# Optimization experiments

Measured on AMD Instinct MI355X. Metric: run time of the kernel, lower is better.

## Reference

```python
import jax, jax.numpy as jnp
import numpy as np

B, T, U, D = 8, 200, 50, 512
INNER, VOCAB = 640, 1024


def setup_inputs() -> dict:
    key = jax.random.key(0)
    k1, k2, k3, k4 = jax.random.split(key, 4)
    enc_outputs = jax.random.normal(k1, (B, T, D), dtype=jnp.float32)
    dec_outputs = jax.random.normal(k2, (B, U, D), dtype=jnp.float32)
    # Dense(inner_dim, activation='tanh') params
    W1 = jax.random.normal(k3, (D, INNER), dtype=jnp.float32) / np.sqrt(D)
    b1 = jnp.zeros((INNER,), dtype=jnp.float32)
    # Dense(vocab_size) params
    W2 = jax.random.normal(k4, (INNER, VOCAB), dtype=jnp.float32) / np.sqrt(INNER)
    b2 = jnp.zeros((VOCAB,), dtype=jnp.float32)
    return {"enc_outputs": enc_outputs, "dec_outputs": dec_outputs,
            "W1": W1, "b1": b1, "W2": W2, "b2": b2}


def reference(enc_outputs, dec_outputs, W1, b1, W2, b2):
    # joint_inputs: (B, T, U, D) via broadcast add, exactly as the TF module
    joint = enc_outputs[:, :, None, :] + dec_outputs[:, None, :, :]
    hidden = jnp.tanh(jnp.einsum('btud,dh->btuh', joint, W1) + b1)  # (B,T,U,INNER)
    logits = jnp.einsum('btuh,hv->btuv', hidden, W2) + b2            # (B,T,U,VOCAB)
    return logits
```

## Files before the change

kernel.cpp:

```cpp
#include <hip/hip_runtime.h>
#include <hip/hip_bf16.h>
#include <stdint.h>

namespace {

constexpr int B = 8, T = 200, U = 50, D = 512, INNER = 640, VOCAB = 1024;
constexpr int M_TOTAL = B * T * U;
constexpr int ROWS_E = B * T;
constexpr int ROWS_D = B * U;
constexpr int ROWS_ED = ROWS_E + ROWS_D;
constexpr int BM = 128, BN = 512;
constexpr int CK = 128;

typedef __bf16 bf16x8 __attribute__((ext_vector_type(8)));
typedef float  f32x4  __attribute__((ext_vector_type(4)));
typedef unsigned short u16;
typedef unsigned int   u32;

constexpr size_t ED_BYTES = (size_t)ROWS_ED * INNER * 4;

__device__ __forceinline__ u16 f2bf(float f) {
  uint32_t u = __float_as_uint(f);
  uint32_t rounding = 0x7FFFu + ((u >> 16) & 1u);
  return (u16)((u + rounding) >> 16);
}

__device__ __forceinline__ float fast_tanh(float x) {
  float e = __expf(2.0f * x);
  float r = __builtin_amdgcn_rcpf(e + 1.0f);
  return 1.0f - 2.0f * r;
}

__global__ __launch_bounds__(320) void k_prep(const float* __restrict__ enc,
                                              const float* __restrict__ dec,
                                              const float* __restrict__ W1,
                                              const float* __restrict__ b1,
                                              const float* __restrict__ W2,
                                              float* __restrict__ ED,
                                              u16* __restrict__ W2B) {
  if (blockIdx.x >= 500) {
    const int idx = (blockIdx.x - 500) * 320 + threadIdx.x;
    const int lane = idx & 63;
    const int f = idx >> 6;
    const int ks = f >> 6;
    const int nf = f & 63;
    const int n = nf * 16 + (lane & 15);
    const int k = ks * 32 + (lane >> 4) * 8;
    u16 v[8];
#pragma unroll
    for (int j = 0; j < 8; ++j)
      v[j] = f2bf(W2[(size_t)(k + j) * VOCAB + n]);
    uint64_t lo = (uint64_t)v[0] | ((uint64_t)v[1] << 16) |
                  ((uint64_t)v[2] << 32) | ((uint64_t)v[3] << 48);
    uint64_t hi = (uint64_t)v[4] | ((uint64_t)v[5] << 16) |
                  ((uint64_t)v[6] << 32) | ((uint64_t)v[7] << 48);
    uint64_t* dst = reinterpret_cast<uint64_t*>(W2B + (size_t)idx * 8);
    dst[0] = lo;
    dst[1] = hi;
    return;
  }

  __shared__ float rows[4 * D];
  const int r0 = blockIdx.x * 4;
  const bool is_enc = (r0 < ROWS_E);
  const float* src = is_enc ? (enc + (size_t)r0 * D)
                            : (dec + (size_t)(r0 - ROWS_E) * D);
  for (int i = threadIdx.x; i < 4 * D; i += 320) rows[i] = src[i];
  __syncthreads();

  const int c0 = threadIdx.x, c1 = threadIdx.x + 320;
  float acc[4][2];
  const float bias0 = is_enc ? b1[c0] : 0.f;
  const float bias1 = is_enc ? b1[c1] : 0.f;
#pragma unroll
  for (int r = 0; r < 4; ++r) { acc[r][0] = bias0; acc[r][1] = bias1; }

  for (int d = 0; d < D; d += 8) {
    f32x4 rv[4][2];
#pragma unroll
    for (int r = 0; r < 4; ++r) {
      rv[r][0] = *reinterpret_cast<const f32x4*>(&rows[r * D + d]);
      rv[r][1] = *reinterpret_cast<const f32x4*>(&rows[r * D + d + 4]);
    }
#pragma unroll
    for (int dd = 0; dd < 8; ++dd) {
      const float w0 = W1[(size_t)(d + dd) * INNER + c0];
      const float w1 = W1[(size_t)(d + dd) * INNER + c1];
#pragma unroll
      for (int r = 0; r < 4; ++r) {
        const float x = rv[r][dd >> 2][dd & 3];
        acc[r][0] = fmaf(x, w0, acc[r][0]);
        acc[r][1] = fmaf(x, w1, acc[r][1]);
      }
    }
  }
#pragma unroll
  for (int r = 0; r < 4; ++r) {
    ED[(size_t)(r0 + r) * INNER + c0] = acc[r][0];
    ED[(size_t)(r0 + r) * INNER + c1] = acc[r][1];
  }
}

__global__ __launch_bounds__(512, 2) void k_main(const float* __restrict__ ED,
                                                 const u16* __restrict__ W2B,
                                                 const float* __restrict__ b2,
                                                 float* __restrict__ out) {
  __shared__ u16 At[2][BM * CK];
  const int tid = threadIdx.x;
  const int m0 = blockIdx.x * BM;
  const int n0 = blockIdx.y * BN;

  const int lane = tid & 63;
  const int wv   = tid >> 6;
  const int llo  = lane & 15;
  const int lhi  = lane >> 4;

  const int trow = wv * 16 + llo;
  const int m = m0 + trow;
  const int bb = m / (T * U);
  const int rem = m - bb * (T * U);
  const int tt = rem / U;
  const int uu = rem - tt * U;
  const float* Erow = ED + (size_t)(bb * T + tt) * INNER;
  const float* Drow = ED + (size_t)(ROWS_E + bb * U + uu) * INNER;
  const int klo = lhi * 8;

  auto tanh_chunk = [&](int c, int bufsel) __attribute__((always_inline)) {
    char* dst = reinterpret_cast<char*>(At[bufsel]) + (wv << 12) + lane * 16;
#pragma unroll
    for (int kq = 0; kq < 4; ++kq) {
      const int k = c * CK + kq * 32 + klo;
      const f32x4 e0 = *reinterpret_cast<const f32x4*>(Erow + k);
      const f32x4 e1 = *reinterpret_cast<const f32x4*>(Erow + k + 4);
      const f32x4 d0 = *reinterpret_cast<const f32x4*>(Drow + k);
      const f32x4 d1 = *reinterpret_cast<const f32x4*>(Drow + k + 4);
      int4 pk;
      pk.x = (int)((u32)f2bf(fast_tanh(e0[0] + d0[0])) |
                   ((u32)f2bf(fast_tanh(e0[1] + d0[1])) << 16));
      pk.y = (int)((u32)f2bf(fast_tanh(e0[2] + d0[2])) |
                   ((u32)f2bf(fast_tanh(e0[3] + d0[3])) << 16));
      pk.z = (int)((u32)f2bf(fast_tanh(e1[0] + d1[0])) |
                   ((u32)f2bf(fast_tanh(e1[1] + d1[1])) << 16));
      pk.w = (int)((u32)f2bf(fast_tanh(e1[2] + d1[2])) |
                   ((u32)f2bf(fast_tanh(e1[3] + d1[3])) << 16));
      *reinterpret_cast<int4*>(dst + (kq << 10)) = pk;
    }
  };

  const u16* Bp = W2B + ((size_t)((n0 >> 4) + wv * 4) << 9) + lane * 8;
  const int albase = lane * 16;

  f32x4 acc[8][4];
#pragma unroll
  for (int mi = 0; mi < 8; ++mi)
#pragma unroll
    for (int ni = 0; ni < 4; ++ni) acc[mi][ni] = (f32x4){0.f, 0.f, 0.f, 0.f};

  tanh_chunk(0, 0);
  bf16x8 bcur[4], bnext[4];
#pragma unroll
  for (int ni = 0; ni < 4; ++ni)
    bcur[ni] = *reinterpret_cast<const bf16x8*>(Bp + ((size_t)ni << 9));
  __syncthreads();

  for (int c = 0; c < 5; ++c) {
    const char* asrc = reinterpret_cast<const char*>(At[c & 1]);
    if (c < 4) tanh_chunk(c + 1, (c + 1) & 1);

#pragma unroll
    for (int kq = 0; kq < 4; ++kq) {
      const int ks = c * 4 + kq;
      if (ks < 19) {
#pragma unroll
        for (int ni = 0; ni < 4; ++ni)
          bnext[ni] = *reinterpret_cast<const bf16x8*>(
              Bp + ((size_t)((ks + 1) * 64 + ni) << 9));
      }
      bf16x8 a[8];
#pragma unroll
      for (int mi = 0; mi < 8; ++mi)
        a[mi] = *reinterpret_cast<const bf16x8*>(
            asrc + (((mi << 2) + kq) << 10) + albase);
#pragma unroll
      for (int mi = 0; mi < 8; ++mi)
#pragma unroll
        for (int ni = 0; ni < 4; ++ni)
          acc[mi][ni] = __builtin_amdgcn_mfma_f32_16x16x32_bf16(a[mi], bcur[ni], acc[mi][ni], 0, 0, 0);
      if (ks < 19) {
#pragma unroll
        for (int ni = 0; ni < 4; ++ni) bcur[ni] = bnext[ni];
      }
    }
    __syncthreads();
  }

  float b2v[4];
#pragma unroll
  for (int ni = 0; ni < 4; ++ni) b2v[ni] = b2[n0 + wv * 64 + ni * 16 + llo];

#pragma unroll
  for (int mi = 0; mi < 8; ++mi) {
#pragma unroll
    for (int q = 0; q < 4; ++q) {
      const int r = m0 + mi * 16 + lhi * 4 + q;
      float* orow = out + (size_t)r * VOCAB + n0 + wv * 64 + llo;
#pragma unroll
      for (int ni = 0; ni < 4; ++ni)
        __builtin_nontemporal_store(acc[mi][ni][q] + b2v[ni], orow + ni * 16);
    }
  }
}

}

extern "C" void kernel_launch(void* const* d_in, const int* in_sizes, int n_in,
                              void* d_out, int out_size, void* d_ws, size_t ws_size,
                              hipStream_t stream) {
  const float* enc = (const float*)d_in[0];
  const float* dec = (const float*)d_in[1];
  const float* W1  = (const float*)d_in[2];
  const float* b1  = (const float*)d_in[3];
  const float* W2  = (const float*)d_in[4];
  const float* b2  = (const float*)d_in[5];
  float* out = (float*)d_out;

  float* ED  = (float*)d_ws;
  u16*   W2B = (u16*)((char*)d_ws + ED_BYTES);

  hipLaunchKernelGGL(k_prep, dim3(756), dim3(320), 0, stream,
                     enc, dec, W1, b1, W2, ED, W2B);
  hipLaunchKernelGGL(k_main, dim3(M_TOTAL / BM, VOCAB / BN), dim3(512), 0, stream,
                     ED, W2B, b2, out);
}
```

Before: 219.5 us.

## Halve main-kernel M tile, raise occupancy, and batch more rows per prep block

The main GEMM kernel's row tile drops from 128 to 64. The tanh/bf16 staging of A is now split across wave pairs, and each wave holds a 4x4 accumulator instead of 8x4. Launch bounds go to 4 blocks per SM, and the register double-buffering of B fragments is removed. This gives twice as many blocks and higher occupancy for latency hiding, at the cost of reading W2 from global memory twice as often per output row. The prep kernel now handles 8 rows per block instead of 4, so each W1 load is reused across more rows.

Result: slower. 235.1 us (+7.1%).

```diff
diff --git a/kernel.cpp b/kernel.cpp
--- a/kernel.cpp
+++ b/kernel.cpp
@@ -9,8 +9,6 @@
 constexpr int ROWS_E = B * T;
 constexpr int ROWS_D = B * U;
 constexpr int ROWS_ED = ROWS_E + ROWS_D;
-constexpr int BM = 128, BN = 512;
-constexpr int CK = 128;
 
 typedef __bf16 bf16x8 __attribute__((ext_vector_type(8)));
 typedef float  f32x4  __attribute__((ext_vector_type(4)));
@@ -38,8 +36,8 @@
                                               const float* __restrict__ W2,
                                               float* __restrict__ ED,
                                               u16* __restrict__ W2B) {
-  if (blockIdx.x >= 500) {
-    const int idx = (blockIdx.x - 500) * 320 + threadIdx.x;
+  if (blockIdx.x >= 250) {
+    const int idx = (blockIdx.x - 250) * 320 + threadIdx.x;
     const int lane = idx & 63;
     const int f = idx >> 6;
     const int ks = f >> 6;
@@ -60,62 +58,66 @@
     return;
   }
 
-  __shared__ float rows[4 * D];
-  const int r0 = blockIdx.x * 4;
+  __shared__ float rows[8 * D];
+  const int r0 = blockIdx.x * 8;
   const bool is_enc = (r0 < ROWS_E);
   const float* src = is_enc ? (enc + (size_t)r0 * D)
                             : (dec + (size_t)(r0 - ROWS_E) * D);
-  for (int i = threadIdx.x; i < 4 * D; i += 320) rows[i] = src[i];
+  for (int i = threadIdx.x; i < 8 * D; i += 320) rows[i] = src[i];
   __syncthreads();
 
   const int c0 = threadIdx.x, c1 = threadIdx.x + 320;
-  float acc[4][2];
+  float acc[8][2];
   const float bias0 = is_enc ? b1[c0] : 0.f;
   const float bias1 = is_enc ? b1[c1] : 0.f;
 #pragma unroll
-  for (int r = 0; r < 4; ++r) { acc[r][0] = bias0; acc[r][1] = bias1; }
-
-  for (int d = 0; d < D; d += 8) {
-    f32x4 rv[4][2];
-#pragma unroll
-    for (int r = 0; r < 4; ++r) {
-      rv[r][0] = *reinterpret_cast<const f32x4*>(&rows[r * D + d]);
-      rv[r][1] = *reinterpret_cast<const f32x4*>(&rows[r * D + d + 4]);
-    }
-#pragma unroll
-    for (int dd = 0; dd < 8; ++dd) {
+  for (int r = 0; r < 8; ++r) { acc[r][0] = bias0; acc[r][1] = bias1; }
+
+  for (int d = 0; d < D; d += 4) {
+    float4 rv[8];
+#pragma unroll
+    for (int r = 0; r < 8; ++r)
+      rv[r] = *reinterpret_cast<const float4*>(&rows[r * D + d]);
+#pragma unroll
+    for (int dd = 0; dd < 4; ++dd) {
       const float w0 = W1[(size_t)(d + dd) * INNER + c0];
       const float w1 = W1[(size_t)(d + dd) * INNER + c1];
 #pragma unroll
-      for (int r = 0; r < 4; ++r) {
-        const float x = rv[r][dd >> 2][dd & 3];
+      for (int r = 0; r < 8; ++r) {
+        const float x = (dd == 0) ? rv[r].x : (dd == 1) ? rv[r].y
+                        : (dd == 2) ? rv[r].z : rv[r].w;
         acc[r][0] = fmaf(x, w0, acc[r][0]);
         acc[r][1] = fmaf(x, w1, acc[r][1]);
       }
     }
   }
 #pragma unroll
-  for (int r = 0; r < 4; ++r) {
+  for (int r = 0; r < 8; ++r) {
     ED[(size_t)(r0 + r) * INNER + c0] = acc[r][0];
     ED[(size_t)(r0 + r) * INNER + c1] = acc[r][1];
   }
 }
 
-__global__ __launch_bounds__(512, 2) void k_main(const float* __restrict__ ED,
+__global__ __launch_bounds__(512, 4) void k_main(const float* __restrict__ ED,
                                                  const u16* __restrict__ W2B,
                                                  const float* __restrict__ b2,
                                                  float* __restrict__ out) {
-  __shared__ u16 At[2][BM * CK];
+  constexpr int CK = 128, NCHUNK = 5, CHUNK_B = 16 * 1024;
+  __shared__ u16 At[2 * CHUNK_B / 2];
+  char* At_b = reinterpret_cast<char*>(At);
+
   const int tid = threadIdx.x;
-  const int m0 = blockIdx.x * BM;
-  const int n0 = blockIdx.y * BN;
+  const int m0 = blockIdx.x * 64;
+  const int n0 = blockIdx.y * 512;
 
   const int lane = tid & 63;
   const int wv   = tid >> 6;
   const int llo  = lane & 15;
   const int lhi  = lane >> 4;
 
-  const int trow = wv * 16 + llo;
+  const int rg  = wv & 3;
+  const int kqb = (wv >> 2) << 1;
+  const int trow = rg * 16 + llo;
   const int m = m0 + trow;
   const int bb = m / (T * U);
   const int rem = m - bb * (T * U);
@@ -126,9 +128,10 @@
   const int klo = lhi * 8;
 
   auto tanh_chunk = [&](int c, int bufsel) __attribute__((always_inline)) {
-    char* dst = reinterpret_cast<char*>(At[bufsel]) + (wv << 12) + lane * 16;
-#pragma unroll
-    for (int kq = 0; kq < 4; ++kq) {
+    char* dst = At_b + bufsel * CHUNK_B + lane * 16;
+#pragma unroll
+    for (int q = 0; q < 2; ++q) {
+      const int kq = kqb + q;
       const int k = c * CK + kq * 32 + klo;
       const f32x4 e0 = *reinterpret_cast<const f32x4*>(Erow + k);
       const f32x4 e1 = *reinterpret_cast<const f32x4*>(Erow + k + 4);
@@ -143,53 +146,40 @@
                    ((u32)f2bf(fast_tanh(e1[1] + d1[1])) << 16));
       pk.w = (int)((u32)f2bf(fast_tanh(e1[2] + d1[2])) |
                    ((u32)f2bf(fast_tanh(e1[3] + d1[3])) << 16));
-      *reinterpret_cast<int4*>(dst + (kq << 10)) = pk;
+      *reinterpret_cast<int4*>(dst + ((rg * 4 + kq) << 10)) = pk;
     }
   };
 
   const u16* Bp = W2B + ((size_t)((n0 >> 4) + wv * 4) << 9) + lane * 8;
-  const int albase = lane * 16;
-
-  f32x4 acc[8][4];
-#pragma unroll
-  for (int mi = 0; mi < 8; ++mi)
+
+  f32x4 acc[4][4];
+#pragma unroll
+  for (int mi = 0; mi < 4; ++mi)
 #pragma unroll
     for (int ni = 0; ni < 4; ++ni) acc[mi][ni] = (f32x4){0.f, 0.f, 0.f, 0.f};
 
   tanh_chunk(0, 0);
-  bf16x8 bcur[4], bnext[4];
-#pragma unroll
-  for (int ni = 0; ni < 4; ++ni)
-    bcur[ni] = *reinterpret_cast<const bf16x8*>(Bp + ((size_t)ni << 9));
   __syncthreads();
 
-  for (int c = 0; c < 5; ++c) {
-    const char* asrc = reinterpret_cast<const char*>(At[c & 1]);
-    if (c < 4) tanh_chunk(c + 1, (c + 1) & 1);
-
-#pragma unroll
-    for (int kq = 0; kq < 4; ++kq) {
-      const int ks = c * 4 + kq;
-      if (ks < 19) {
+  for (int c = 0; c < NCHUNK; ++c) {
+    const int ab = (c & 1) * CHUNK_B;
+    if (c < NCHUNK - 1) tanh_chunk(c + 1, (c + 1) & 1);
+#pragma unroll
+    for (int ks = 0; ks < 4; ++ks) {
+      bf16x8 bfr[4], a[4];
+#pragma unroll
+      for (int ni = 0; ni < 4; ++ni)
+        bfr[ni] = *reinterpret_cast<const bf16x8*>(
+            Bp + ((size_t)((c * 4 + ks) * 64 + ni) << 9));
+#pragma unroll
+      for (int mi = 0; mi < 4; ++mi)
+        a[mi] = *reinterpret_cast<const bf16x8*>(
+            At_b + ab + ((mi * 4 + ks) << 10) + lane * 16);
+#pragma unroll
+      for (int mi = 0; mi < 4; ++mi)
 #pragma unroll
         for (int ni = 0; ni < 4; ++ni)
-          bnext[ni] = *reinterpret_cast<const bf16x8*>(
-              Bp + ((size_t)((ks + 1) * 64 + ni) << 9));
-      }
-      bf16x8 a[8];
-#pragma unroll
-      for (int mi = 0; mi < 8; ++mi)
-        a[mi] = *reinterpret_cast<const bf16x8*>(
-            asrc + (((mi << 2) + kq) << 10) + albase);
-#pragma unroll
-      for (int mi = 0; mi < 8; ++mi)
-#pragma unroll
-        for (int ni = 0; ni < 4; ++ni)
-          acc[mi][ni] = __builtin_amdgcn_mfma_f32_16x16x32_bf16(a[mi], bcur[ni], acc[mi][ni], 0, 0, 0);
-      if (ks < 19) {
-#pragma unroll
-        for (int ni = 0; ni < 4; ++ni) bcur[ni] = bnext[ni];
-      }
+          acc[mi][ni] = __builtin_amdgcn_mfma_f32_16x16x32_bf16(a[mi], bfr[ni], acc[mi][ni], 0, 0, 0);
     }
     __syncthreads();
   }
@@ -199,11 +189,11 @@
   for (int ni = 0; ni < 4; ++ni) b2v[ni] = b2[n0 + wv * 64 + ni * 16 + llo];
 
 #pragma unroll
-  for (int mi = 0; mi < 8; ++mi) {
+  for (int mi = 0; mi < 4; ++mi) {
 #pragma unroll
     for (int q = 0; q < 4; ++q) {
-      const int r = m0 + mi * 16 + lhi * 4 + q;
-      float* orow = out + (size_t)r * VOCAB + n0 + wv * 64 + llo;
+      const int row = m0 + mi * 16 + lhi * 4 + q;
+      float* orow = out + (size_t)row * VOCAB + n0 + wv * 64 + llo;
 #pragma unroll
       for (int ni = 0; ni < 4; ++ni)
         __builtin_nontemporal_store(acc[mi][ni][q] + b2v[ni], orow + ni * 16);
@@ -227,8 +217,8 @@
   float* ED  = (float*)d_ws;
   u16*   W2B = (u16*)((char*)d_ws + ED_BYTES);
 
-  hipLaunchKernelGGL(k_prep, dim3(756), dim3(320), 0, stream,
+  hipLaunchKernelGGL(k_prep, dim3(506), dim3(320), 0, stream,
                      enc, dec, W1, b1, W2, ED, W2B);
-  hipLaunchKernelGGL(k_main, dim3(M_TOTAL / BM, VOCAB / BN), dim3(512), 0, stream,
-                     ED, W2B, b2, out);
-}
+  hipLaunchKernelGGL(k_main, dim3(M_TOTAL / 64, VOCAB / 512), dim3(512),
+                     0, stream, ED, W2B, b2, out);
+}
```
